# Kernel tuning notes

Hardware: AMD Instinct MI355X
Metric: run time of the kernel (lower is better)

Reference implementation:

```python
import jax, jax.numpy as jnp
from jax import lax
import numpy as np

B, T = 2, 4096
NQ, NAUX, NR, NS, K = 256, 28, 512, 256, 2
DIL = [2 ** i for i in range(10)] * 3  # 30 residual blocks
L = len(DIL)


def _causal_conv(x, w, b, d):
    # x: (B, Cin, T), w: (Cout, Cin, K) -- left-pad (K-1)*d for causality
    pad = (w.shape[-1] - 1) * d
    y = lax.conv_general_dilated(x, w, window_strides=(1,), padding=[(pad, 0)],
                                 rhs_dilation=(d,),
                                 dimension_numbers=('NCH', 'OIH', 'NCH'))
    return y + b[None, :, None]


def _conv1x1(x, w, b):
    # x: (B, Cin, T), w: (Cout, Cin)
    return jnp.einsum('oc,bct->bot', w, x) + b[None, :, None]


def setup_inputs() -> dict:
    key = jax.random.key(0)
    ks = jax.random.split(key, 32)
    s = 0.05
    n = lambda k, shp: (jax.random.normal(k, shp, dtype=jnp.float32) * s)
    return {
        'x': jax.random.randint(ks[0], (B, T), 0, NQ, dtype=jnp.int32),
        'h': jax.random.normal(ks[1], (B, NAUX, T), dtype=jnp.float32),
        'causal_w': n(ks[2], (NR, NQ, K)), 'causal_b': n(ks[3], (NR,)),
        'dil_sig_w': n(ks[4], (L, NR, NR, K)), 'dil_sig_b': n(ks[5], (L, NR)),
        'dil_tanh_w': n(ks[6], (L, NR, NR, K)), 'dil_tanh_b': n(ks[7], (L, NR)),
        'aux_sig_w': n(ks[8], (L, NR, NAUX)), 'aux_sig_b': n(ks[9], (L, NR)),
        'aux_tanh_w': n(ks[10], (L, NR, NAUX)), 'aux_tanh_b': n(ks[11], (L, NR)),
        'skip_w': n(ks[12], (L, NS, NR)), 'skip_b': n(ks[13], (L, NS)),
        'res_w': n(ks[14], (L, NR, NR)), 'res_b': n(ks[15], (L, NR)),
        'post1_w': n(ks[16], (NS, NS)), 'post1_b': n(ks[17], (NS,)),
        'post2_w': n(ks[18], (NQ, NS)), 'post2_b': n(ks[19], (NQ,)),
        'lin_w': n(ks[20], (NQ, NQ)), 'lin_b': n(ks[21], (NQ,)),
    }


def reference(x, h, causal_w, causal_b, dil_sig_w, dil_sig_b, dil_tanh_w,
              dil_tanh_b, aux_sig_w, aux_sig_b, aux_tanh_w, aux_tanh_b,
              skip_w, skip_b, res_w, res_b, post1_w, post1_b, post2_w,
              post2_b, lin_w, lin_b):
    # preprocess: one-hot -> (B, NQ, T) -> causal conv
    oh = jax.nn.one_hot(x % NQ, NQ, dtype=jnp.float32).transpose(0, 2, 1)
    out = _causal_conv(oh, causal_w, causal_b, 1)  # (B, NR, T)
    skip_sum = jnp.zeros((B, NS, T), dtype=jnp.float32)
    for l, d in enumerate(DIL):
        s = _causal_conv(out, dil_sig_w[l], dil_sig_b[l], d) \
            + _conv1x1(h, aux_sig_w[l], aux_sig_b[l])
        t = _causal_conv(out, dil_tanh_w[l], dil_tanh_b[l], d) \
            + _conv1x1(h, aux_tanh_w[l], aux_tanh_b[l])
        g = jax.nn.sigmoid(s) * jnp.tanh(t)  # gated activation (B, NR, T)
        skip_sum = skip_sum + _conv1x1(g, skip_w[l], skip_b[l])
        out = _conv1x1(g, res_w[l], res_b[l]) + out  # residual
    o = jax.nn.relu(skip_sum)
    o = jax.nn.relu(_conv1x1(o, post1_w, post1_b))
    o = _conv1x1(o, post2_w, post2_b).transpose(0, 2, 1)  # (B, T, NQ)
    return o @ lin_w.T + lin_b
```

## Files before the change

kernel.cpp:

```cpp
#include <hip/hip_runtime.h>
#include <cstddef>

#define B_ 2
#define T_ 4096
#define NQ_ 256
#define NAUX_ 28
#define NR_ 512
#define NS_ 256
#define L_ 30

typedef _Float16 half_t;
typedef __attribute__((ext_vector_type(8))) _Float16 f16x8;
typedef __attribute__((ext_vector_type(4))) _Float16 f16x4;
typedef __attribute__((ext_vector_type(4))) float f32x4;

__device__ inline half_t f2h(float f) { return (half_t)f; }
__device__ inline float h2f(half_t h) { return (float)h; }

__device__ __forceinline__ void gload16(const void* g, void* l) {
    __builtin_amdgcn_global_load_lds(
        (const __attribute__((address_space(1))) unsigned int*)g,
        (__attribute__((address_space(3))) unsigned int*)l, 16, 0, 0);
}

__device__ __forceinline__ void phase_barrier() {
    asm volatile("" ::: "memory");
    __builtin_amdgcn_s_barrier();
    asm volatile("" ::: "memory");
}
__device__ __forceinline__ void gate_barrier() {
    asm volatile("s_waitcnt vmcnt(6)" ::: "memory");
    __builtin_amdgcn_s_barrier();
    asm volatile("" ::: "memory");
}


__global__ __launch_bounds__(512, 2) void gates8(
    const half_t* __restrict__ actB, const half_t* __restrict__ Wf,
    const float* __restrict__ biasG, half_t* __restrict__ g,
    const half_t* __restrict__ zbuf, int dil)
{
    __shared__ __align__(16) half_t sA[3][16 * 512];
    __shared__ __align__(16) half_t sB[3][256 * 64];

    const int tid = threadIdx.x;
    const int b = blockIdx.z;
    const int tB = blockIdx.x * 256;
    const int w = tid >> 6, lane = tid & 63;
    const int wm = w >> 2, wn = w & 3;
    const int l15 = lane & 15, lg = lane >> 4;
    const int rr = lane >> 3, cc = lane & 7;
    const int sc8 = cc ^ rr;
    const int mgB = blockIdx.y * 8;

    f32x4 acc[4][4] = {};
    f16x8 af[4][2];

    auto stageA = [&](int v, int buf) {
#pragma unroll
        for (int s2 = 0; s2 < 2; s2++)
            gload16(&Wf[((size_t)(mgB + w) * 34 + v * 2 + s2) * 512 + lane * 8],
                    &sA[buf][(w * 2 + s2) * 512]);
    };
    auto stageB = [&](int v, int buf) {
#pragma unroll
        for (int it = 0; it < 4; it++) {
            const int t = tB + w * 32 + it * 8 + rr;
            const half_t* p;
            if (v < 8) {
                p = actB + ((size_t)b * T_ + t) * 576 + v * 64;
            } else if (v < 16) {
                const int tp = t - dil;
                p = (tp >= 0) ? actB + ((size_t)b * T_ + tp) * 576 + (v - 8) * 64
                              : zbuf;
            } else {
                p = actB + ((size_t)b * T_ + t) * 576 + 512;
            }
            gload16(p + sc8 * 8, &sB[buf][(w * 32 + it * 8) * 64]);
        }
    };
    auto loadAfrag = [&](int buf) {
#pragma unroll
        for (int i = 0; i < 4; i++)
#pragma unroll
            for (int s = 0; s < 2; s++)
                af[i][s] = *(const f16x8*)&sA[buf][((wm * 4 + i) * 2 + s) * 512 + lane * 8];
    };
    auto loadBfrag = [&](f16x8* bv, int s, int buf) {
#pragma unroll
        for (int j = 0; j < 4; j++) {
            const int r = wn * 64 + j * 16 + l15;
            bv[j] = *(const f16x8*)&sB[buf][r * 64 + (((s * 4 + lg) ^ (l15 & 7)) * 8)];
        }
    };
    auto mfma16 = [&](const f16x8* bv, int s) {
        __builtin_amdgcn_s_setprio(1);
#pragma unroll
        for (int i = 0; i < 4; i++)
#pragma unroll
            for (int j = 0; j < 4; j++)
                acc[i][j] = __builtin_amdgcn_mfma_f32_16x16x32_f16(af[i][s], bv[j], acc[i][j], 0, 0, 0);
        __builtin_amdgcn_s_setprio(0);
    };

    stageA(0, 0); stageB(0, 0);
    stageA(1, 1); stageB(1, 1);
    asm volatile("s_waitcnt vmcnt(6)" ::: "memory");
    __builtin_amdgcn_s_barrier();
    asm volatile("" ::: "memory");

    int buf = 0, nbuf = 2;
    for (int t = 0; t < 17; t++) {
        loadAfrag(buf);
        f16x8 bv0[4];
        loadBfrag(bv0, 0, buf);
        if (t + 2 < 17) stageA(t + 2, nbuf);
        phase_barrier();
        mfma16(bv0, 0);
        f16x8 bv1[4];
        loadBfrag(bv1, 1, buf);
        if (t + 2 < 17) stageB(t + 2, nbuf);
        gate_barrier();
        mfma16(bv1, 1);
        buf = (buf == 2) ? 0 : buf + 1;
        nbuf = (nbuf == 2) ? 0 : nbuf + 1;
    }

    const int gidx = blockIdx.y * 2 + wm;
    const int t0 = tB + wn * 64 + l15;
#pragma unroll
    for (int i = 0; i < 2; i++) {
        const int c = gidx * 32 + i * 16 + lg * 4;
        const float4 bs = *(const float4*)&biasG[gidx * 64 + i * 16 + lg * 4];
        const float4 bt4 = *(const float4*)&biasG[gidx * 64 + 32 + i * 16 + lg * 4];
        const float bsa[4] = {bs.x, bs.y, bs.z, bs.w};
        const float bta[4] = {bt4.x, bt4.y, bt4.z, bt4.w};
#pragma unroll
        for (int j = 0; j < 4; j++) {
            const int t = t0 + j * 16;
            f16x4 o;
#pragma unroll
            for (int e = 0; e < 4; e++) {
                const float sv = acc[i][j][e] + bsa[e];
                const float tv = acc[i + 2][j][e] + bta[e];
                const float sg = 1.f / (1.f + __expf(-sv));
                const float ex = __expf(-2.f * tv);
                const float th = (1.f - ex) / (1.f + ex);
                o[e] = f2h(sg * th);
            }
            *(f16x4*)(g + ((size_t)b * T_ + t) * 512 + c) = o;
        }
    }
}

__global__ __launch_bounds__(512, 2) void res8(
    const half_t* __restrict__ X, const half_t* __restrict__ Wf,
    const float* __restrict__ bias, half_t* __restrict__ actB,
    half_t* __restrict__ skipH)
{
    __shared__ __align__(16) half_t sA[3][16 * 512];
    __shared__ __align__(16) half_t sB[3][256 * 64];

    const int tid = threadIdx.x;
    const int b = blockIdx.z;
    const int tB = blockIdx.x * 256;
    const int mB = blockIdx.y * 128;
    const int w = tid >> 6, lane = tid & 63;
    const int wm = w >> 2, wn = w & 3;
    const int l15 = lane & 15, lg = lane >> 4;
    const int rr = lane >> 3, cc = lane & 7;
    const int sc8 = cc ^ rr;
    const int mgB = blockIdx.y * 8;

    f32x4 acc[4][4] = {};
    f16x8 af[4][2];

    const half_t* Xb = X + ((size_t)b * T_ + tB) * 512;

    auto stageA = [&](int v, int buf) {
#pragma unroll
        for (int s2 = 0; s2 < 2; s2++)
            gload16(&Wf[((size_t)(mgB + w) * 16 + v * 2 + s2) * 512 + lane * 8],
                    &sA[buf][(w * 2 + s2) * 512]);
    };
    auto stageB = [&](int v, int buf) {
#pragma unroll
        for (int it = 0; it < 4; it++) {
            const int row = w * 32 + it * 8;
            gload16(Xb + (size_t)(row + rr) * 512 + v * 64 + sc8 * 8,
                    &sB[buf][row * 64]);
        }
    };
    auto loadAfrag = [&](int buf) {
#pragma unroll
        for (int i = 0; i < 4; i++)
#pragma unroll
            for (int s = 0; s < 2; s++)
                af[i][s] = *(const f16x8*)&sA[buf][((wm * 4 + i) * 2 + s) * 512 + lane * 8];
    };
    auto loadBfrag = [&](f16x8* bv, int s, int buf) {
#pragma unroll
        for (int j = 0; j < 4; j++) {
            const int r = wn * 64 + j * 16 + l15;
            bv[j] = *(const f16x8*)&sB[buf][r * 64 + (((s * 4 + lg) ^ (l15 & 7)) * 8)];
        }
    };
    auto mfma16 = [&](const f16x8* bv, int s) {
        __builtin_amdgcn_s_setprio(1);
#pragma unroll
        for (int i = 0; i < 4; i++)
#pragma unroll
            for (int j = 0; j < 4; j++)
                acc[i][j] = __builtin_amdgcn_mfma_f32_16x16x32_f16(af[i][s], bv[j], acc[i][j], 0, 0, 0);
        __builtin_amdgcn_s_setprio(0);
    };

    stageA(0, 0); stageB(0, 0);
    stageA(1, 1); stageB(1, 1);
    asm volatile("s_waitcnt vmcnt(6)" ::: "memory");
    __builtin_amdgcn_s_barrier();
    asm volatile("" ::: "memory");

    int buf = 0, nbuf = 2;
    for (int t = 0; t < 8; t++) {
        loadAfrag(buf);
        f16x8 bv0[4];
        loadBfrag(bv0, 0, buf);
        if (t + 2 < 8) stageA(t + 2, nbuf);
        phase_barrier();
        mfma16(bv0, 0);
        f16x8 bv1[4];
        loadBfrag(bv1, 1, buf);
        if (t + 2 < 8) stageB(t + 2, nbuf);
        gate_barrier();
        mfma16(bv1, 1);
        buf = (buf == 2) ? 0 : buf + 1;
        nbuf = (nbuf == 2) ? 0 : nbuf + 1;
    }

    const int n0 = tB + wn * 64 + l15;
#pragma unroll
    for (int i = 0; i < 4; i++) {
        const int m = mB + wm * 64 + i * 16 + lg * 4;
        const float4 bv = *(const float4*)&bias[m];
#pragma unroll
        for (int j = 0; j < 4; j++) {
            const int t = n0 + j * 16;
            const float o0 = acc[i][j][0] + bv.x, o1 = acc[i][j][1] + bv.y;
            const float o2 = acc[i][j][2] + bv.z, o3 = acc[i][j][3] + bv.w;
            const size_t bt = (size_t)b * T_ + t;
            half_t* p = (mB + wm * 64 + i * 16 < 512)
                            ? (actB + bt * 576 + m)
                            : (skipH + bt * 256 + (m - 512));
            f16x4 old = *(const f16x4*)p;
            f16x4 nv = {f2h(h2f(old.x) + o0), f2h(h2f(old.y) + o1),
                        f2h(h2f(old.z) + o2), f2h(h2f(old.w) + o3)};
            *(f16x4*)p = nv;
        }
    }
}

template<int K, int EPI>
__global__ __launch_bounds__(256, 2) void gemm_mfma(
    const half_t* __restrict__ X, const half_t* __restrict__ Wf,
    const float* __restrict__ bias, void* __restrict__ out, int M,
    half_t* __restrict__ actB, half_t* __restrict__ skipH)
{
    constexpr int NITER = K / 128;
    constexpr int NKS = K / 32;
    __shared__ __align__(16) half_t sB[2][256 * 64];

    const int tid = threadIdx.x;
    const int b = blockIdx.z;
    const int tB = blockIdx.x * 128;
    const int mB = blockIdx.y * 128;
    const int w = tid >> 6, lane = tid & 63;
    const int wm = w >> 1, wn = w & 1;
    const int l15 = lane & 15, lg = lane >> 4;
    const int rr = lane >> 3, cc = lane & 7;
    const int sc8 = cc ^ rr;

    f32x4 acc[4][4] = {};
    f16x8 aC[8], aP[8];

    const int mgW = (mB >> 4) + wm * 4;
    const half_t* Xb = X + ((size_t)b * T_ + tB) * K;

    auto loadA = [&](f16x8* d, int v) {
#pragma unroll
        for (int i = 0; i < 4; i++)
#pragma unroll
            for (int s = 0; s < 2; s++)
                d[i * 2 + s] = *(const f16x8*)&Wf[((size_t)(mgW + i) * NKS + v * 2 + s) * 512 + lane * 8];
    };
    auto stageSlice = [&](int v, int rowbase, int buf) {
#pragma unroll
        for (int it = 0; it < 4; it++) {
            const int row = w * 32 + it * 8;
            gload16(Xb + (size_t)(row + rr) * K + v * 64 + sc8 * 8,
                    &sB[buf][(rowbase + row) * 64]);
        }
    };
    auto compute = [&](const f16x8* a, int rowbase, int buf) {
#pragma unroll
        for (int s = 0; s < 2; s++) {
            f16x8 bv[4];
#pragma unroll
            for (int j = 0; j < 4; j++) {
                const int r = rowbase + wn * 64 + j * 16 + l15;
                bv[j] = *(const f16x8*)&sB[buf][r * 64 + (((s * 4 + lg) ^ (l15 & 7)) * 8)];
            }
#pragma unroll
            for (int i = 0; i < 4; i++)
#pragma unroll
                for (int j = 0; j < 4; j++)
                    acc[i][j] = __builtin_amdgcn_mfma_f32_16x16x32_f16(a[i * 2 + s], bv[j], acc[i][j], 0, 0, 0);
        }
    };

    stageSlice(0, 0, 0);
    stageSlice(1, 128, 0);
    loadA(aC, 0);
    loadA(aP, 1);
#pragma unroll
    for (int kc = 0; kc < NITER; kc++) {
        __syncthreads();
        if (kc + 1 < NITER) {
            stageSlice(2 * kc + 2, 0, (kc + 1) & 1);
            stageSlice(2 * kc + 3, 128, (kc + 1) & 1);
        }
        compute(aC, 0, kc & 1);
        if (kc + 1 < NITER) loadA(aC, 2 * kc + 2);
        compute(aP, 128, kc & 1);
        if (kc + 1 < NITER) loadA(aP, 2 * kc + 3);
    }

    const int n0 = tB + wn * 64 + l15;
#pragma unroll
    for (int i = 0; i < 4; i++) {
        const int m = mB + wm * 64 + i * 16 + lg * 4;
        float4 bv = make_float4(0.f, 0.f, 0.f, 0.f);
        if (bias) bv = *(const float4*)&bias[m];
#pragma unroll
        for (int j = 0; j < 4; j++) {
            const int t = n0 + j * 16;
            float o0 = acc[i][j][0] + bv.x, o1 = acc[i][j][1] + bv.y;
            float o2 = acc[i][j][2] + bv.z, o3 = acc[i][j][3] + bv.w;
            if (EPI == 1) {
                o0 = fmaxf(o0, 0.f); o1 = fmaxf(o1, 0.f);
                o2 = fmaxf(o2, 0.f); o3 = fmaxf(o3, 0.f);
            }
            if (EPI == 3) {
                const size_t bt = (size_t)b * T_ + t;
                half_t* p = (mB < 512) ? (actB + bt * 576 + m)
                                       : (skipH + bt * 256 + (m - 512));
                f16x4 old = *(const f16x4*)p;
                f16x4 nv = {f2h(h2f(old.x) + o0), f2h(h2f(old.y) + o1),
                            f2h(h2f(old.z) + o2), f2h(h2f(old.w) + o3)};
                *(f16x4*)p = nv;
            } else {
                const size_t off = ((size_t)b * T_ + t) * M + m;
                if (EPI == 2) {
                    *(float4*)((float*)out + off) = make_float4(o0, o1, o2, o3);
                } else {
                    f16x4 ov = {f2h(o0), f2h(o1), f2h(o2), f2h(o3)};
                    *(f16x4*)((half_t*)out + off) = ov;
                }
            }
        }
    }
}

__global__ __launch_bounds__(256) void relupack_kernel(
    const half_t* __restrict__ skipH, half_t* __restrict__ outp)
{
    const int idx = blockIdx.x * 256 + threadIdx.x;
    const int c = (idx & 63) * 4;
    const int bt = idx >> 6;
    const f16x4 v = *(const f16x4*)(skipH + (size_t)bt * 256 + c);
    f16x4 o = {f2h(fmaxf(h2f(v.x), 0.f)), f2h(fmaxf(h2f(v.y), 0.f)),
               f2h(fmaxf(h2f(v.z), 0.f)), f2h(fmaxf(h2f(v.w), 0.f))};
    *(f16x4*)(outp + (size_t)bt * 256 + c) = o;
}

__global__ __launch_bounds__(256) void embed_kernel(
    const int* __restrict__ x, const float* __restrict__ cw,
    const float* __restrict__ cb, half_t* __restrict__ actB)
{
    const int t = blockIdx.x, b = blockIdx.y;
    const int idc = x[b * T_ + t];
    const int idp = (t > 0) ? x[b * T_ + t - 1] : -1;
    const size_t bt = (size_t)b * T_ + t;
    for (int c = threadIdx.x; c < 512; c += 256) {
        float v = cw[(c * 256 + idc) * 2 + 1] + cb[c];
        if (idp >= 0) v += cw[(c * 256 + idp) * 2 + 0];
        actB[bt * 576 + c] = f2h(v);
    }
}

__global__ __launch_bounds__(256) void packh_kernel(
    const float* __restrict__ h, half_t* __restrict__ actB)
{
    const int idx = blockIdx.x * 256 + threadIdx.x;
    const int j = idx & 63;
    const int bt = idx >> 6;
    const int b = bt >> 12, t = bt & 4095;
    const float v = (j < 28) ? h[((size_t)b * NAUX_ + j) * T_ + t] : 0.f;
    actB[(size_t)bt * 576 + 512 + j] = f2h(v);
}

__global__ __launch_bounds__(256) void packgate_kernel(
    const float* __restrict__ dsw, const float* __restrict__ dtw,
    half_t* __restrict__ Wg)
{
    const int idx = blockIdx.x * 256 + threadIdx.x;
    const int lane = idx & 63;
    const int ks = (idx >> 6) & 15;
    const int mg = (idx >> 10) & 63;
    const int l = idx >> 16;
    const int r = mg * 16 + (lane & 15);
    const int rsub = r & 63;
    const int c = (r >> 6) * 32 + (rsub & 31);
    const float* src = (rsub < 32) ? dsw : dtw;
    const size_t base = ((size_t)(l * 512 + c) * 512 + ks * 32 + (lane >> 4) * 8) * 2;
    const float4* p = (const float4*)(src + base);
    const float4 q0 = p[0], q1 = p[1], q2 = p[2], q3 = p[3];
    f16x8 cur = {f2h(q0.y), f2h(q0.w), f2h(q1.y), f2h(q1.w),
                 f2h(q2.y), f2h(q2.w), f2h(q3.y), f2h(q3.w)};
    f16x8 pst = {f2h(q0.x), f2h(q0.z), f2h(q1.x), f2h(q1.z),
                 f2h(q2.x), f2h(q2.z), f2h(q3.x), f2h(q3.z)};
    half_t* dst = Wg + (size_t)l * 1114112;
    *(f16x8*)&dst[((size_t)(mg * 34 + ks) * 64 + lane) * 8] = cur;
    *(f16x8*)&dst[((size_t)(mg * 34 + 16 + ks) * 64 + lane) * 8] = pst;
}

__global__ __launch_bounds__(256) void packgaux_kernel(
    const float* __restrict__ asw, const float* __restrict__ atw,
    half_t* __restrict__ Wg)
{
    const int idx = blockIdx.x * 256 + threadIdx.x;
    const int lane = idx & 63;
    const int ksd = (idx >> 6) & 1;
    const int mg = (idx >> 7) & 63;
    const int l = idx >> 13;
    const int r = mg * 16 + (lane & 15);
    const int rsub = r & 63;
    const int c = (r >> 6) * 32 + (rsub & 31);
    const float* src = (rsub < 32) ? asw : atw;
    const int j0 = ksd * 32 + (lane >> 4) * 8;
    f16x8 v = {};
#pragma unroll
    for (int e = 0; e < 8; e++) {
        const int j = j0 + e;
        if (j < NAUX_) v[e] = f2h(src[(size_t)(l * 512 + c) * NAUX_ + j]);
    }
    Wg += (size_t)l * 1114112;
    *(f16x8*)&Wg[((size_t)(mg * 34 + 32 + ksd) * 64 + lane) * 8] = v;
}

__global__ __launch_bounds__(256) void packsr_kernel(
    const float* __restrict__ rsw, const float* __restrict__ skw,
    half_t* __restrict__ Wsr)
{
    const int idx = blockIdx.x * 256 + threadIdx.x;
    const int lane = idx & 63;
    const int ks = (idx >> 6) & 15;
    const int mg = (idx >> 10) % 48;
    const int l = (idx >> 10) / 48;
    const int r = mg * 16 + (lane & 15);
    const int kb = ks * 32 + (lane >> 4) * 8;
    const float* src = (r < 512) ? (rsw + ((size_t)l * 512 + r) * 512 + kb)
                                 : (skw + ((size_t)l * 256 + (r - 512)) * 512 + kb);
    const float4 q0 = ((const float4*)src)[0], q1 = ((const float4*)src)[1];
    f16x8 v = {f2h(q0.x), f2h(q0.y), f2h(q0.z), f2h(q0.w),
               f2h(q1.x), f2h(q1.y), f2h(q1.z), f2h(q1.w)};
    *(f16x8*)&Wsr[(size_t)l * 393216 + ((size_t)(mg * 16 + ks) * 64 + lane) * 8] = v;
}

__global__ __launch_bounds__(256) void packpost_kernel(
    const float* __restrict__ p1w, const float* __restrict__ p2w,
    const float* __restrict__ lw, half_t* __restrict__ Wpost)
{
    const int idx = blockIdx.x * 256 + threadIdx.x;
    const int lane = idx & 63;
    const int ks = (idx >> 6) & 7;
    const int mg = (idx >> 9) & 15;
    const int mi = idx >> 13;
    const float* src = (mi == 0) ? p1w : (mi == 1) ? p2w : lw;
    const int r = mg * 16 + (lane & 15);
    const int kb = ks * 32 + (lane >> 4) * 8;
    const float4 q0 = ((const float4*)(src + (size_t)r * 256 + kb))[0];
    const float4 q1 = ((const float4*)(src + (size_t)r * 256 + kb))[1];
    f16x8 v = {f2h(q0.x), f2h(q0.y), f2h(q0.z), f2h(q0.w),
               f2h(q1.x), f2h(q1.y), f2h(q1.z), f2h(q1.w)};
    *(f16x8*)&Wpost[(size_t)mi * 65536 + ((size_t)(mg * 8 + ks) * 64 + lane) * 8] = v;
}

__global__ __launch_bounds__(256) void packbias_kernel(
    const float* __restrict__ dsb, const float* __restrict__ asb,
    const float* __restrict__ dtb, const float* __restrict__ atb,
    const float* __restrict__ rsb, const float* __restrict__ skb,
    float* __restrict__ biasG, float* __restrict__ biasSr)
{
    const int idx = blockIdx.x * 256 + threadIdx.x;
    if (idx < 30 * 1024) {
        const int l = idx >> 10, r = idx & 1023;
        const int rsub = r & 63;
        const int c = (r >> 6) * 32 + (rsub & 31);
        const float v = (rsub < 32) ? (dsb[l * 512 + c] + asb[l * 512 + c])
                                    : (dtb[l * 512 + c] + atb[l * 512 + c]);
        biasG[idx] = v;
    } else if (idx < 30 * 1024 + 30 * 768) {
        const int j = idx - 30 * 1024;
        const int l = j / 768, r = j % 768;
        biasSr[j] = (r < 512) ? rsb[l * 512 + r] : skb[l * 256 + (r - 512)];
    }
}

extern "C" void kernel_launch(void* const* d_in, const int* in_sizes, int n_in,
                              void* d_out, int out_size, void* d_ws, size_t ws_size,
                              hipStream_t stream)
{
    (void)in_sizes; (void)n_in; (void)out_size; (void)ws_size;

    const int* x = (const int*)d_in[0];
    const float* h = (const float*)d_in[1];
    const float* causal_w = (const float*)d_in[2];
    const float* causal_b = (const float*)d_in[3];
    const float* dsw = (const float*)d_in[4];
    const float* dsb = (const float*)d_in[5];
    const float* dtw = (const float*)d_in[6];
    const float* dtb = (const float*)d_in[7];
    const float* asw = (const float*)d_in[8];
    const float* asb = (const float*)d_in[9];
    const float* atw = (const float*)d_in[10];
    const float* atb = (const float*)d_in[11];
    const float* skw = (const float*)d_in[12];
    const float* skb = (const float*)d_in[13];
    const float* rsw = (const float*)d_in[14];
    const float* rsb = (const float*)d_in[15];
    const float* p1w = (const float*)d_in[16];
    const float* p1b = (const float*)d_in[17];
    const float* p2w = (const float*)d_in[18];
    const float* p2b = (const float*)d_in[19];
    const float* lw  = (const float*)d_in[20];
    const float* lb  = (const float*)d_in[21];

    char* ws = (char*)d_ws;
    size_t off = 0;
    auto alloc = [&](size_t bytes) { char* p = ws + off; off += (bytes + 255) & ~(size_t)255; return p; };

    half_t* Wg     = (half_t*)alloc((size_t)L_ * 1114112 * 2);
    half_t* Wsr    = (half_t*)alloc((size_t)L_ * 393216 * 2);
    half_t* Wpost  = (half_t*)alloc((size_t)3 * 65536 * 2);
    float*  biasG  = (float*) alloc((size_t)L_ * 1024 * 4);
    float*  biasSr = (float*) alloc((size_t)L_ * 768 * 4);
    half_t* actB   = (half_t*)alloc((size_t)B_ * T_ * 576 * 2);
    half_t* g      = (half_t*)alloc((size_t)B_ * T_ * 512 * 2);
    half_t* skipH  = (half_t*)alloc((size_t)B_ * T_ * 256 * 2);
    half_t* zbuf   = (half_t*)alloc(256);
    half_t* pA     = (half_t*)alloc((size_t)B_ * T_ * 256 * 2);
    half_t* pB     = (half_t*)alloc((size_t)B_ * T_ * 256 * 2);

    hipMemsetAsync(skipH, 0, (size_t)B_ * T_ * 256 * 2 + 256, stream);

    packgate_kernel<<<30 * 64 * 16 * 64 / 256, 256, 0, stream>>>(dsw, dtw, Wg);
    packgaux_kernel<<<30 * 64 * 2 * 64 / 256, 256, 0, stream>>>(asw, atw, Wg);
    packsr_kernel<<<30 * 48 * 16 * 64 / 256, 256, 0, stream>>>(rsw, skw, Wsr);
    packpost_kernel<<<3 * 16 * 8 * 64 / 256, 256, 0, stream>>>(p1w, p2w, lw, Wpost);
    packbias_kernel<<<(30 * 1024 + 30 * 768 + 255) / 256, 256, 0, stream>>>(
        dsb, asb, dtb, atb, rsb, skb, biasG, biasSr);
    packh_kernel<<<B_ * T_ * 64 / 256, 256, 0, stream>>>(h, actB);
    embed_kernel<<<dim3(T_, B_), 256, 0, stream>>>(x, causal_w, causal_b, actB);

    for (int l = 0; l < L_; l++) {
        const int dil = 1 << (l % 10);
        gates8<<<dim3(16, 8, B_), 512, 0, stream>>>(
            actB, Wg + (size_t)l * 1114112, biasG + (size_t)l * 1024, g, zbuf, dil);
        res8<<<dim3(16, 6, B_), 512, 0, stream>>>(
            g, Wsr + (size_t)l * 393216, biasSr + (size_t)l * 768, actB, skipH);
    }

    relupack_kernel<<<B_ * T_ * 64 / 256, 256, 0, stream>>>(skipH, pA);
    gemm_mfma<256, 1><<<dim3(32, 2, B_), 256, 0, stream>>>(pA, Wpost, p1b, pB, 256,
                                                           nullptr, nullptr);
    gemm_mfma<256, 0><<<dim3(32, 2, B_), 256, 0, stream>>>(pB, Wpost + 65536, p2b, pA, 256,
                                                           nullptr, nullptr);
    gemm_mfma<256, 2><<<dim3(32, 2, B_), 256, 0, stream>>>(pA, Wpost + 131072, lb, d_out, 256,
                                                           nullptr, nullptr);
}
```

Before: 1.475 ms.

## Remap GEMM blocks for XCD-local weight reuse and coalesce weight packing via LDS

The gates8 and res8 kernels now remap the hardware block index so that blocks landing on the same XCD (round-robin by index mod 8) share the same output-channel weight slice across different time tiles. The aim is to improve L2 reuse of weights within each XCD. Separately, the gate and residual/skip weight packing kernels are rewritten so each block reads full contiguous weight rows with coalesced float4 loads, transposes them through LDS, and writes the packed fp16 layout. This replaces scattered per-thread strided reads. The remap relies on the assumption that the hardware dispatches blocks to XCDs round-robin by linear index.

```diff
diff --git a/kernel.cpp b/kernel.cpp
--- a/kernel.cpp
+++ b/kernel.cpp
@@ -12,6 +12,7 @@
 typedef _Float16 half_t;
 typedef __attribute__((ext_vector_type(8))) _Float16 f16x8;
 typedef __attribute__((ext_vector_type(4))) _Float16 f16x4;
+typedef __attribute__((ext_vector_type(2))) _Float16 f16x2;
 typedef __attribute__((ext_vector_type(4))) float f32x4;
 
 __device__ inline half_t f2h(float f) { return (half_t)f; }
@@ -44,14 +45,19 @@
     __shared__ __align__(16) half_t sB[3][256 * 64];
 
     const int tid = threadIdx.x;
-    const int b = blockIdx.z;
-    const int tB = blockIdx.x * 256;
+    const int hw = blockIdx.x + 16 * (blockIdx.y + 8 * blockIdx.z);
+    const int xcd = hw & 7;
+    const int jj = hw >> 3;
+    const int yv = jj & 7;
+    const int tBz = xcd + 8 * ((jj >> 3) & 3);
+    const int b = tBz >> 4;
+    const int tB = (tBz & 15) * 256;
     const int w = tid >> 6, lane = tid & 63;
     const int wm = w >> 2, wn = w & 3;
     const int l15 = lane & 15, lg = lane >> 4;
     const int rr = lane >> 3, cc = lane & 7;
     const int sc8 = cc ^ rr;
-    const int mgB = blockIdx.y * 8;
+    const int mgB = yv * 8;
 
     f32x4 acc[4][4] = {};
     f16x8 af[4][2];
@@ -126,7 +132,7 @@
         nbuf = (nbuf == 2) ? 0 : nbuf + 1;
     }
 
-    const int gidx = blockIdx.y * 2 + wm;
+    const int gidx = yv * 2 + wm;
     const int t0 = tB + wn * 64 + l15;
 #pragma unroll
     for (int i = 0; i < 2; i++) {
@@ -162,15 +168,20 @@
     __shared__ __align__(16) half_t sB[3][256 * 64];
 
     const int tid = threadIdx.x;
-    const int b = blockIdx.z;
-    const int tB = blockIdx.x * 256;
-    const int mB = blockIdx.y * 128;
+    const int hw = blockIdx.x + 16 * (blockIdx.y + 6 * blockIdx.z);
+    const int xcd = hw & 7;
+    const int jj = hw >> 3;
+    const int yv = jj % 6;
+    const int tBz = xcd + 8 * (jj / 6);
+    const int b = tBz >> 4;
+    const int tB = (tBz & 15) * 256;
+    const int mB = yv * 128;
     const int w = tid >> 6, lane = tid & 63;
     const int wm = w >> 2, wn = w & 3;
     const int l15 = lane & 15, lg = lane >> 4;
     const int rr = lane >> 3, cc = lane & 7;
     const int sc8 = cc ^ rr;
-    const int mgB = blockIdx.y * 8;
+    const int mgB = yv * 8;
 
     f32x4 acc[4][4] = {};
     f16x8 af[4][2];
@@ -413,25 +424,33 @@
     const float* __restrict__ dsw, const float* __restrict__ dtw,
     half_t* __restrict__ Wg)
 {
-    const int idx = blockIdx.x * 256 + threadIdx.x;
-    const int lane = idx & 63;
-    const int ks = (idx >> 6) & 15;
-    const int mg = (idx >> 10) & 63;
-    const int l = idx >> 16;
-    const int r = mg * 16 + (lane & 15);
-    const int rsub = r & 63;
-    const int c = (r >> 6) * 32 + (rsub & 31);
-    const float* src = (rsub < 32) ? dsw : dtw;
-    const size_t base = ((size_t)(l * 512 + c) * 512 + ks * 32 + (lane >> 4) * 8) * 2;
-    const float4* p = (const float4*)(src + base);
-    const float4 q0 = p[0], q1 = p[1], q2 = p[2], q3 = p[3];
-    f16x8 cur = {f2h(q0.y), f2h(q0.w), f2h(q1.y), f2h(q1.w),
-                 f2h(q2.y), f2h(q2.w), f2h(q3.y), f2h(q3.w)};
-    f16x8 pst = {f2h(q0.x), f2h(q0.z), f2h(q1.x), f2h(q1.z),
-                 f2h(q2.x), f2h(q2.z), f2h(q3.x), f2h(q3.z)};
-    half_t* dst = Wg + (size_t)l * 1114112;
-    *(f16x8*)&dst[((size_t)(mg * 34 + ks) * 64 + lane) * 8] = cur;
-    *(f16x8*)&dst[((size_t)(mg * 34 + 16 + ks) * 64 + lane) * 8] = pst;
+    __shared__ half_t lds[16 * 1040];
+    const int mg = blockIdx.x;
+    const int l  = blockIdx.y;
+    const int tid = threadIdx.x;
+    const int rsub0 = (mg * 16) & 63;
+    const int c0 = ((mg * 16) >> 6) * 32 + (rsub0 & 31);
+    const float* src = ((rsub0 < 32) ? dsw : dtw) + ((size_t)(l * 512 + c0)) * 1024;
+    const int row = tid >> 4, gq = tid & 15;
+    const float4* srow = (const float4*)(src + (size_t)row * 1024);
+#pragma unroll
+    for (int u = 0; u < 16; u++) {
+        const int q = u * 16 + gq;
+        const float4 v = srow[q];
+        *(f16x2*)&lds[row * 1040 + 2 * q]       = f16x2{f2h(v.x), f2h(v.z)};
+        *(f16x2*)&lds[row * 1040 + 512 + 2 * q] = f16x2{f2h(v.y), f2h(v.w)};
+    }
+    __syncthreads();
+    const int lane = tid & 63, wv = tid >> 6;
+    half_t* dst = Wg + (size_t)l * 1114112 + (size_t)mg * 34 * 512;
+#pragma unroll
+    for (int v = 0; v < 8; v++) {
+        const int s = wv + 4 * v;
+        const int tap = (s < 16) ? 1 : 0;
+        const f16x8 val = *(const f16x8*)&lds[(lane & 15) * 1040 + tap * 512
+                                              + (s & 15) * 32 + (lane >> 4) * 8];
+        *(f16x8*)&dst[((size_t)s * 64 + lane) * 8] = val;
+    }
 }
 
 __global__ __launch_bounds__(256) void packgaux_kernel(
@@ -462,19 +481,31 @@
     const float* __restrict__ rsw, const float* __restrict__ skw,
     half_t* __restrict__ Wsr)
 {
-    const int idx = blockIdx.x * 256 + threadIdx.x;
-    const int lane = idx & 63;
-    const int ks = (idx >> 6) & 15;
-    const int mg = (idx >> 10) % 48;
-    const int l = (idx >> 10) / 48;
-    const int r = mg * 16 + (lane & 15);
-    const int kb = ks * 32 + (lane >> 4) * 8;
-    const float* src = (r < 512) ? (rsw + ((size_t)l * 512 + r) * 512 + kb)
-                                 : (skw + ((size_t)l * 256 + (r - 512)) * 512 + kb);
-    const float4 q0 = ((const float4*)src)[0], q1 = ((const float4*)src)[1];
-    f16x8 v = {f2h(q0.x), f2h(q0.y), f2h(q0.z), f2h(q0.w),
-               f2h(q1.x), f2h(q1.y), f2h(q1.z), f2h(q1.w)};
-    *(f16x8*)&Wsr[(size_t)l * 393216 + ((size_t)(mg * 16 + ks) * 64 + lane) * 8] = v;
+    __shared__ half_t lds[16 * 520];
+    const int mg = blockIdx.x;
+    const int l  = blockIdx.y;
+    const int tid = threadIdx.x;
+    const int r0 = mg * 16;
+    const float* src = (r0 < 512) ? (rsw + ((size_t)l * 512 + r0) * 512)
+                                  : (skw + ((size_t)l * 256 + (r0 - 512)) * 512);
+    const int row = tid >> 4, gq = tid & 15;
+    const float4* srow = (const float4*)(src + (size_t)row * 512);
+#pragma unroll
+    for (int u = 0; u < 8; u++) {
+        const int q = u * 16 + gq;
+        const float4 v = srow[q];
+        f16x4 h4 = {f2h(v.x), f2h(v.y), f2h(v.z), f2h(v.w)};
+        *(f16x4*)&lds[row * 520 + 4 * q] = h4;
+    }
+    __syncthreads();
+    const int lane = tid & 63, wv = tid >> 6;
+    half_t* dst = Wsr + (size_t)l * 393216 + (size_t)mg * 16 * 512;
+#pragma unroll
+    for (int v = 0; v < 4; v++) {
+        const int s = wv + 4 * v;
+        const f16x8 val = *(const f16x8*)&lds[(lane & 15) * 520 + s * 32 + (lane >> 4) * 8];
+        *(f16x8*)&dst[((size_t)s * 64 + lane) * 8] = val;
+    }
 }
 
 __global__ __launch_bounds__(256) void packpost_kernel(
@@ -564,9 +595,9 @@
 
     hipMemsetAsync(skipH, 0, (size_t)B_ * T_ * 256 * 2 + 256, stream);
 
-    packgate_kernel<<<30 * 64 * 16 * 64 / 256, 256, 0, stream>>>(dsw, dtw, Wg);
+    packgate_kernel<<<dim3(64, 30), 256, 0, stream>>>(dsw, dtw, Wg);
     packgaux_kernel<<<30 * 64 * 2 * 64 / 256, 256, 0, stream>>>(asw, atw, Wg);
-    packsr_kernel<<<30 * 48 * 16 * 64 / 256, 256, 0, stream>>>(rsw, skw, Wsr);
+    packsr_kernel<<<dim3(48, 30), 256, 0, stream>>>(rsw, skw, Wsr);
     packpost_kernel<<<3 * 16 * 8 * 64 / 256, 256, 0, stream>>>(p1w, p2w, lw, Wpost);
     packbias_kernel<<<(30 * 1024 + 30 * 768 + 255) / 256, 256, 0, stream>>>(
         dsb, asb, dtb, atb, rsb, skb, biasG, biasSr);
```

Result: slower. 1.513 ms (+2.6%).
